# Performance work log

Measured on AMD Instinct MI355X. Metric: run time of the kernel, lower is better.

The kernel has to match this reference:

```python
import jax, jax.numpy as jnp
import numpy as np

MARGIN = 1.0


def setup_inputs() -> dict:
    key = jax.random.key(0)
    k1, k2 = jax.random.split(key)
    inputs = jax.random.normal(k1, (512, 256), dtype=jnp.float32)
    targets = jax.random.randint(k2, (512,), 0, 64)
    return {"inputs": inputs, "targets": targets}


def reference(inputs, targets):
    n = inputs.shape[0]
    # pairwise euclidean distance matrix [n, n]
    sq = jnp.sum(inputs * inputs, axis=1)
    dist = sq[:, None] + sq[None, :] - 2.0 * (inputs @ inputs.T)
    dist = jnp.sqrt(jnp.clip(dist, 1e-16))

    # triplet margins: ap_dist[i,j] - an_dist[i,k] + margin -> [n, n, n]
    triplet = dist[:, :, None] - dist[:, None, :] + MARGIN

    # mask: i != j, i != k, j != k, labels[i]==labels[j], labels[i]!=labels[k]
    not_eye = ~jnp.eye(n, dtype=bool)
    dist_idx = not_eye[:, :, None] & not_eye[:, None, :] & not_eye[None, :, :]
    teq = targets[:, None] == targets[None, :]  # symmetric [n, n]
    valid = teq[:, :, None] & (~teq[:, None, :])
    mask = (valid & dist_idx).astype(triplet.dtype)

    triplet = jnp.maximum(mask * triplet, 0.0)
    num_triplets = jnp.sum((triplet > 1e-16).astype(triplet.dtype))
    return jnp.sum(triplet) / (num_triplets + 1e-16)
```

## Files before the change

### kernel.cpp

```cpp
#include <hip/hip_runtime.h>

constexpr int N = 512;
constexpr int D = 256;
#define MARGIN 1.0f

__global__ __launch_bounds__(1024, 8) void triplet_fused(
    const float* __restrict__ x, const int* __restrict__ tgt,
    float* __restrict__ part) {
  __shared__ __align__(16) float m[N];
  __shared__ float clist[N];
  __shared__ int nv;
  __shared__ float wred[32];

  const int i = blockIdx.x;
  const int tid = threadIdx.x;
  const int ti = tgt[i];
  const int wave = tid >> 6, lane = tid & 63;
  const int sub = lane & 15, rg = lane >> 4;

  if (tid == 0) nv = 0;

  const float4* xiv = (const float4*)(x + (size_t)i * D);
  float4 a0 = xiv[sub];
  float4 a1 = xiv[16 + sub];
  float4 a2 = xiv[32 + sub];
  float4 a3 = xiv[48 + sub];
  __syncthreads();

  const int rot = (i * 171) & (N - 1);
  const int rbase = wave * 32 + rg;
  #pragma unroll 2
  for (int it = 0; it < 8; ++it) {
    const int r = (rbase + it * 4 + rot) & (N - 1);
    const float4* xr = (const float4*)(x + (size_t)r * D);
    float4 b0 = xr[sub];
    float4 b1 = xr[16 + sub];
    float4 b2 = xr[32 + sub];
    float4 b3 = xr[48 + sub];
    float4 e0, e1, e2, e3;
    e0.x = a0.x - b0.x; e0.y = a0.y - b0.y; e0.z = a0.z - b0.z; e0.w = a0.w - b0.w;
    e1.x = a1.x - b1.x; e1.y = a1.y - b1.y; e1.z = a1.z - b1.z; e1.w = a1.w - b1.w;
    e2.x = a2.x - b2.x; e2.y = a2.y - b2.y; e2.z = a2.z - b2.z; e2.w = a2.w - b2.w;
    e3.x = a3.x - b3.x; e3.y = a3.y - b3.y; e3.z = a3.z - b3.z; e3.w = a3.w - b3.w;
    float s01 = e0.x*e0.x + e0.y*e0.y + e0.z*e0.z + e0.w*e0.w
              + e1.x*e1.x + e1.y*e1.y + e1.z*e1.z + e1.w*e1.w;
    float s23 = e2.x*e2.x + e2.y*e2.y + e2.z*e2.z + e2.w*e2.w
              + e3.x*e3.x + e3.y*e3.y + e3.z*e3.z + e3.w*e3.w;
    float s = s01 + s23;
    #pragma unroll
    for (int off = 8; off > 0; off >>= 1) s += __shfl_down(s, off);
    if (sub == 0) {
      float d = sqrtf(fmaxf(s, 1e-16f));
      int tj = tgt[r];
      m[r] = (tj != ti) ? d : __builtin_inff();
      if (tj == ti && r != i) {
        int sl = atomicAdd(&nv, 1);
        clist[sl] = d + MARGIN;
      }
    }
  }
  __syncthreads();

  float sum = 0.f, cnt = 0.f;
  const int e = tid & 511, half = tid >> 9;
  const float mk = m[e];
  const int n = nv;
  for (int v = half; v < n; v += 2) {
    float a = clist[v] - mk;
    sum += fmaxf(a, 0.f);
    cnt += (a > 1e-16f ? 1.f : 0.f);
  }

  #pragma unroll
  for (int off = 32; off > 0; off >>= 1) {
    sum += __shfl_down(sum, off);
    cnt += __shfl_down(cnt, off);
  }
  if (lane == 0) { wred[wave] = sum; wred[16 + wave] = cnt; }
  __syncthreads();
  if (tid == 0) {
    float s = 0.f, c = 0.f;
    #pragma unroll
    for (int w = 0; w < 16; ++w) { s += wred[w]; c += wred[16 + w]; }
    part[2 * i] = s;
    part[2 * i + 1] = c;
  }
}

__global__ __launch_bounds__(512) void triplet_finalize(
    const float* __restrict__ part, float* __restrict__ out) {
  __shared__ float wred[16];
  const int tid = threadIdx.x;
  float s = part[2 * tid], c = part[2 * tid + 1];
  #pragma unroll
  for (int off = 32; off > 0; off >>= 1) {
    s += __shfl_down(s, off);
    c += __shfl_down(c, off);
  }
  int wave = tid >> 6, lane = tid & 63;
  if (lane == 0) { wred[wave] = s; wred[8 + wave] = c; }
  __syncthreads();
  if (tid == 0) {
    float ts = 0.f, tc = 0.f;
    #pragma unroll
    for (int w = 0; w < 8; ++w) { ts += wred[w]; tc += wred[8 + w]; }
    out[0] = ts / (tc + 1e-16f);
  }
}

extern "C" void kernel_launch(void* const* d_in, const int* in_sizes, int n_in,
                              void* d_out, int out_size, void* d_ws, size_t ws_size,
                              hipStream_t stream) {
  const float* x = (const float*)d_in[0];
  const int* tgt = (const int*)d_in[1];
  float* out = (float*)d_out;
  float* part = (float*)d_ws;

  triplet_fused<<<N, 1024, 0, stream>>>(x, tgt, part);
  triplet_finalize<<<1, 512, 0, stream>>>(part, out);
}
```

Before: 67.75 us.

## Process two anchor rows per block to reuse loaded rows

Each block now handles two anchors instead of one, so every row of x loaded from memory feeds two distance computations. The grid halves to 256 blocks and the finalize kernel shrinks to match. This cuts global and L2 row traffic and per-block overhead. The cost is more registers per thread, a longer serial triplet loop per block, and fewer blocks to spread across the MI355X's CUs.

```diff
diff --git a/kernel.cpp b/kernel.cpp
--- a/kernel.cpp
+++ b/kernel.cpp
@@ -4,30 +4,35 @@
 constexpr int D = 256;
 #define MARGIN 1.0f
 
-__global__ __launch_bounds__(1024, 8) void triplet_fused(
+#define ACC(S, A, B)                                                   \
+  { float ex = A.x - B.x, ey = A.y - B.y, ez = A.z - B.z,              \
+          ew = A.w - B.w;                                              \
+    S += ex * ex + ey * ey + ez * ez + ew * ew; }
+
+__global__ __launch_bounds__(1024, 4) void triplet_fused(
     const float* __restrict__ x, const int* __restrict__ tgt,
     float* __restrict__ part) {
-  __shared__ __align__(16) float m[N];
-  __shared__ float clist[N];
-  __shared__ int nv;
+  __shared__ __align__(16) float m0[N], m1[N];
+  __shared__ float cl0[N], cl1[N];
+  __shared__ int nv0, nv1;
   __shared__ float wred[32];
 
-  const int i = blockIdx.x;
+  const int b = blockIdx.x;
+  const int i0 = 2 * b, i1 = 2 * b + 1;
   const int tid = threadIdx.x;
-  const int ti = tgt[i];
   const int wave = tid >> 6, lane = tid & 63;
   const int sub = lane & 15, rg = lane >> 4;
+  const int t0 = tgt[i0], t1 = tgt[i1];
 
-  if (tid == 0) nv = 0;
+  if (tid == 0) { nv0 = 0; nv1 = 0; }
 
-  const float4* xiv = (const float4*)(x + (size_t)i * D);
-  float4 a0 = xiv[sub];
-  float4 a1 = xiv[16 + sub];
-  float4 a2 = xiv[32 + sub];
-  float4 a3 = xiv[48 + sub];
+  const float4* xa = (const float4*)(x + (size_t)i0 * D);
+  const float4* xc = (const float4*)(x + (size_t)i1 * D);
+  float4 a0 = xa[sub], a1 = xa[16 + sub], a2 = xa[32 + sub], a3 = xa[48 + sub];
+  float4 c0 = xc[sub], c1 = xc[16 + sub], c2 = xc[32 + sub], c3 = xc[48 + sub];
   __syncthreads();
 
-  const int rot = (i * 171) & (N - 1);
+  const int rot = (b * 171) & (N - 1);
   const int rbase = wave * 32 + rg;
   #pragma unroll 2
   for (int it = 0; it < 8; ++it) {
@@ -37,36 +42,37 @@
     float4 b1 = xr[16 + sub];
     float4 b2 = xr[32 + sub];
     float4 b3 = xr[48 + sub];
-    float4 e0, e1, e2, e3;
-    e0.x = a0.x - b0.x; e0.y = a0.y - b0.y; e0.z = a0.z - b0.z; e0.w = a0.w - b0.w;
-    e1.x = a1.x - b1.x; e1.y = a1.y - b1.y; e1.z = a1.z - b1.z; e1.w = a1.w - b1.w;
-    e2.x = a2.x - b2.x; e2.y = a2.y - b2.y; e2.z = a2.z - b2.z; e2.w = a2.w - b2.w;
-    e3.x = a3.x - b3.x; e3.y = a3.y - b3.y; e3.z = a3.z - b3.z; e3.w = a3.w - b3.w;
-    float s01 = e0.x*e0.x + e0.y*e0.y + e0.z*e0.z + e0.w*e0.w
-              + e1.x*e1.x + e1.y*e1.y + e1.z*e1.z + e1.w*e1.w;
-    float s23 = e2.x*e2.x + e2.y*e2.y + e2.z*e2.z + e2.w*e2.w
-              + e3.x*e3.x + e3.y*e3.y + e3.z*e3.z + e3.w*e3.w;
-    float s = s01 + s23;
+    float sa = 0.f, sb = 0.f;
+    ACC(sa, a0, b0); ACC(sa, a1, b1); ACC(sa, a2, b2); ACC(sa, a3, b3);
+    ACC(sb, c0, b0); ACC(sb, c1, b1); ACC(sb, c2, b2); ACC(sb, c3, b3);
     #pragma unroll
-    for (int off = 8; off > 0; off >>= 1) s += __shfl_down(s, off);
+    for (int off = 8; off > 0; off >>= 1) {
+      sa += __shfl_down(sa, off);
+      sb += __shfl_down(sb, off);
+    }
     if (sub == 0) {
-      float d = sqrtf(fmaxf(s, 1e-16f));
-      int tj = tgt[r];
-      m[r] = (tj != ti) ? d : __builtin_inff();
-      if (tj == ti && r != i) {
-        int sl = atomicAdd(&nv, 1);
-        clist[sl] = d + MARGIN;
-      }
+      const int tj = tgt[r];
+      float da = sqrtf(fmaxf(sa, 1e-16f));
+      float db = sqrtf(fmaxf(sb, 1e-16f));
+      m0[r] = (tj != t0) ? da : __builtin_inff();
+      m1[r] = (tj != t1) ? db : __builtin_inff();
+      if (tj == t0 && r != i0) { int s = atomicAdd(&nv0, 1); cl0[s] = da + MARGIN; }
+      if (tj == t1 && r != i1) { int s = atomicAdd(&nv1, 1); cl1[s] = db + MARGIN; }
     }
   }
   __syncthreads();
 
   float sum = 0.f, cnt = 0.f;
   const int e = tid & 511, half = tid >> 9;
-  const float mk = m[e];
-  const int n = nv;
-  for (int v = half; v < n; v += 2) {
-    float a = clist[v] - mk;
+  const float mk0 = m0[e], mk1 = m1[e];
+  const int n0 = nv0, n1 = nv1;
+  for (int v = half; v < n0; v += 2) {
+    float a = cl0[v] - mk0;
+    sum += fmaxf(a, 0.f);
+    cnt += (a > 1e-16f ? 1.f : 0.f);
+  }
+  for (int v = half; v < n1; v += 2) {
+    float a = cl1[v] - mk1;
     sum += fmaxf(a, 0.f);
     cnt += (a > 1e-16f ? 1.f : 0.f);
   }
@@ -82,14 +88,14 @@
     float s = 0.f, c = 0.f;
     #pragma unroll
     for (int w = 0; w < 16; ++w) { s += wred[w]; c += wred[16 + w]; }
-    part[2 * i] = s;
-    part[2 * i + 1] = c;
+    part[2 * b] = s;
+    part[2 * b + 1] = c;
   }
 }
 
-__global__ __launch_bounds__(512) void triplet_finalize(
+__global__ __launch_bounds__(256) void triplet_finalize(
     const float* __restrict__ part, float* __restrict__ out) {
-  __shared__ float wred[16];
+  __shared__ float wred[8];
   const int tid = threadIdx.x;
   float s = part[2 * tid], c = part[2 * tid + 1];
   #pragma unroll
@@ -98,12 +104,11 @@
     c += __shfl_down(c, off);
   }
   int wave = tid >> 6, lane = tid & 63;
-  if (lane == 0) { wred[wave] = s; wred[8 + wave] = c; }
+  if (lane == 0) { wred[wave] = s; wred[4 + wave] = c; }
   __syncthreads();
   if (tid == 0) {
-    float ts = 0.f, tc = 0.f;
-    #pragma unroll
-    for (int w = 0; w < 8; ++w) { ts += wred[w]; tc += wred[8 + w]; }
+    float ts = wred[0] + wred[1] + wred[2] + wred[3];
+    float tc = wred[4] + wred[5] + wred[6] + wred[7];
     out[0] = ts / (tc + 1e-16f);
   }
 }
@@ -116,6 +121,6 @@
   float* out = (float*)d_out;
   float* part = (float*)d_ws;
 
-  triplet_fused<<<N, 1024, 0, stream>>>(x, tgt, part);
-  triplet_finalize<<<1, 512, 0, stream>>>(part, out);
+  triplet_fused<<<N / 2, 1024, 0, stream>>>(x, tgt, part);
+  triplet_finalize<<<1, 256, 0, stream>>>(part, out);
 }
```

After: 66.49 us. About the same (-1.9%).
